# Kernel optimization log

Measured on AMD Instinct MI355X. Metric: run time of the kernel, lower is better.

Reference implementation:

```python
import jax, jax.numpy as jnp
import numpy as np

N_REP = 8      # N: repeated gelu(LN(linear)) blocks
M_LAYERS = 4   # M: transformer encoder layers
SEQ = 100
D = 4
FF = 2048      # PyTorch TransformerEncoderLayer default dim_feedforward
H = 4          # nhead; head_dim = 1


def _ln(x, g, b, axes):
    m = jnp.mean(x, axis=axes, keepdims=True)
    v = jnp.var(x, axis=axes, keepdims=True)
    return (x - m) / jnp.sqrt(v + 1e-5) * g + b


def _encoder_layer(x, Win, bi, Wout, bout, W1, b1, W2, b2, g1, be1, g2, be2):
    # x: [S, Nb, D] with S = batch_size (batch_first=False!), Nb = 100
    S, Nb, E = x.shape
    qkv = x @ Win.T + bi                      # [S, Nb, 3D]
    q, k, v = jnp.split(qkv, 3, axis=-1)
    qh = q.reshape(S, Nb, H, E // H)          # head_dim = 1, scale 1/sqrt(1)=1
    kh = k.reshape(S, Nb, H, E // H)
    vh = v.reshape(S, Nb, H, E // H)
    scores = jnp.einsum('snhd,tnhd->nhst', qh, kh)   # [Nb, H, S, S]
    attn = jax.nn.softmax(scores, axis=-1)
    o = jnp.einsum('nhst,tnhd->snhd', attn, vh).reshape(S, Nb, E)
    o = o @ Wout.T + bout
    x = _ln(x + o, g1, be1, (-1,))            # post-norm (norm_first=False)
    f = jax.nn.relu(x @ W1.T + b1) @ W2.T + b2
    return _ln(x + f, g2, be2, (-1,))


def setup_inputs() -> dict:
    key = jax.random.key(0)
    ks = jax.random.split(key, 24)
    B = 256
    d = {}
    d['x'] = jax.random.normal(ks[0], (B, SEQ, D), dtype=jnp.float32)
    # conv1: kernel_size=1, 1->1 channel -> scalar affine
    d['conv_w'] = jax.random.normal(ks[1], (), dtype=jnp.float32) * 0.5 + 1.0
    d['conv_b'] = jax.random.normal(ks[2], (), dtype=jnp.float32) * 0.1
    # shared 4x4 linear (self.liner) and LayerNorm([100,4])
    d['Wl'] = jax.random.normal(ks[3], (D, D), dtype=jnp.float32) * 0.5
    d['bl'] = jax.random.normal(ks[4], (D,), dtype=jnp.float32) * 0.1
    d['ln_g'] = jnp.ones((SEQ, D), dtype=jnp.float32)
    d['ln_b'] = jnp.zeros((SEQ, D), dtype=jnp.float32)
    # transformer encoder params, stacked over M layers
    s = 0.3
    d['Win'] = jax.random.normal(ks[5], (M_LAYERS, 3 * D, D), dtype=jnp.float32) * s
    d['bi'] = jax.random.normal(ks[6], (M_LAYERS, 3 * D), dtype=jnp.float32) * 0.05
    d['Wout'] = jax.random.normal(ks[7], (M_LAYERS, D, D), dtype=jnp.float32) * s
    d['bout'] = jax.random.normal(ks[8], (M_LAYERS, D), dtype=jnp.float32) * 0.05
    d['W1'] = jax.random.normal(ks[9], (M_LAYERS, FF, D), dtype=jnp.float32) * 0.05
    d['b1'] = jax.random.normal(ks[10], (M_LAYERS, FF), dtype=jnp.float32) * 0.05
    d['W2'] = jax.random.normal(ks[11], (M_LAYERS, D, FF), dtype=jnp.float32) * 0.02
    d['b2'] = jax.random.normal(ks[12], (M_LAYERS, D), dtype=jnp.float32) * 0.05
    d['g1'] = jnp.ones((M_LAYERS, D), dtype=jnp.float32)
    d['be1'] = jnp.zeros((M_LAYERS, D), dtype=jnp.float32)
    d['g2'] = jnp.ones((M_LAYERS, D), dtype=jnp.float32)
    d['be2'] = jnp.zeros((M_LAYERS, D), dtype=jnp.float32)
    return d


def reference(x, conv_w, conv_b, Wl, bl, ln_g, ln_b,
              Win, bi, Wout, bout, W1, b1, W2, b2, g1, be1, g2, be2):
    # per-channel kernel_size=1 conv == elementwise affine (same scalar for all 4 channels)
    h = x * conv_w + conv_b                   # [B, 100, 4]
    for _ in range(N_REP):
        h = jax.nn.gelu(_ln(h @ Wl.T + bl, ln_g, ln_b, (-2, -1)), approximate=False)
    h = h @ Wl.T + bl
    for i in range(M_LAYERS):
        h = _encoder_layer(h, Win[i], bi[i], Wout[i], bout[i], W1[i], b1[i],
                           W2[i], b2[i], g1[i], be1[i], g2[i], be2[i])
    h = h @ Wl.T + bl
    return jax.nn.softmax(h, axis=2)
```

## Files before the change

kernel.cpp:

```cpp
#include <hip/hip_runtime.h>
#include <math.h>

#define SEQ   100
#define BATCH 256
#define NREP  8
#define FFD   2048
#define RSQRT2 0.70710678118654752440f

__device__ __forceinline__ float wsum(float v) {
#pragma unroll
  for (int o = 32; o > 0; o >>= 1) v += __shfl_xor(v, o, 64);
  return v;
}

__global__ __launch_bounds__(64) void k_stageA(
    const float* __restrict__ x, const float* __restrict__ convw,
    const float* __restrict__ convb, const float* __restrict__ Wl,
    const float* __restrict__ bl, const float* __restrict__ lng,
    const float* __restrict__ lnb, float* __restrict__ XT)
{
  const int b = blockIdx.x;
  const int lane = threadIdx.x;
  const bool act = lane < 50;

  const float cw = convw[0], cb = convb[0];
  float W[4][4], B[4];
#pragma unroll
  for (int j = 0; j < 4; ++j) {
    B[j] = bl[j];
#pragma unroll
    for (int d = 0; d < 4; ++d) W[j][d] = Wl[j * 4 + d];
  }

  float h[2][4] = {{0.f,0.f,0.f,0.f},{0.f,0.f,0.f,0.f}};
  float gg[2][4] = {{0.f}}, eb[2][4] = {{0.f}};
  if (act) {
#pragma unroll
    for (int p = 0; p < 2; ++p) {
      const int r = lane * 2 + p;
      float4 xr = *(const float4*)(x + (b * SEQ + r) * 4);
      h[p][0] = fmaf(xr.x, cw, cb); h[p][1] = fmaf(xr.y, cw, cb);
      h[p][2] = fmaf(xr.z, cw, cb); h[p][3] = fmaf(xr.w, cw, cb);
      float4 gv = *(const float4*)(lng + r * 4);
      float4 bv = *(const float4*)(lnb + r * 4);
      gg[p][0] = gv.x; gg[p][1] = gv.y; gg[p][2] = gv.z; gg[p][3] = gv.w;
      eb[p][0] = bv.x; eb[p][1] = bv.y; eb[p][2] = bv.z; eb[p][3] = bv.w;
    }
  }
  for (int it = 0; it < NREP; ++it) {
    float y[2][4] = {{0.f,0.f,0.f,0.f},{0.f,0.f,0.f,0.f}};
    float s1 = 0.f, s2 = 0.f;
    if (act) {
#pragma unroll
      for (int p = 0; p < 2; ++p)
#pragma unroll
        for (int j = 0; j < 4; ++j) {
          float yy = B[j];
#pragma unroll
          for (int d = 0; d < 4; ++d) yy = fmaf(h[p][d], W[j][d], yy);
          y[p][j] = yy; s1 += yy; s2 = fmaf(yy, yy, s2);
        }
    }
    s1 = wsum(s1); s2 = wsum(s2);
    const float mean = s1 * (1.0f / 400.0f);
    const float var  = s2 * (1.0f / 400.0f) - mean * mean;
    const float rstd = rsqrtf(var + 1e-5f);
    if (act) {
#pragma unroll
      for (int p = 0; p < 2; ++p)
#pragma unroll
        for (int j = 0; j < 4; ++j) {
          float vv = fmaf((y[p][j] - mean) * rstd, gg[p][j], eb[p][j]);
          h[p][j] = 0.5f * vv * (1.0f + erff(vv * RSQRT2));
        }
    }
  }
  if (act) {
#pragma unroll
    for (int p = 0; p < 2; ++p) {
      const int r = lane * 2 + p;
      float yy[4];
#pragma unroll
      for (int j = 0; j < 4; ++j) {
        float a = B[j];
#pragma unroll
        for (int d = 0; d < 4; ++d) a = fmaf(h[p][d], W[j][d], a);
        yy[j] = a;
      }
      *(float4*)(XT + (r * BATCH + b) * 4) =
          make_float4(yy[0], yy[1], yy[2], yy[3]);
    }
  }
}

__global__ __launch_bounds__(512) void k_layer(
    const float* __restrict__ XTin, float* __restrict__ XTout,
    const float* __restrict__ Wa,  const float* __restrict__ ba,
    const float* __restrict__ Wo,  const float* __restrict__ bo,
    const float* __restrict__ W1l, const float* __restrict__ b1l,
    const float* __restrict__ W2l, const float* __restrict__ b2l,
    const float* __restrict__ g1l, const float* __restrict__ e1l,
    const float* __restrict__ g2l, const float* __restrict__ e2l,
    const float* __restrict__ Wl,  const float* __restrict__ bl,
    float* __restrict__ out, const int last)
{
  const int n      = blockIdx.x;
  const int base_s = blockIdx.y * 128;
  const int t      = threadIdx.x;
  const int lane   = t & 63;
  const int wv     = t >> 6;
  const int h      = t >> 7;
  const int qr     = t & 127;

  __shared__ float2 kv[4][256];
  __shared__ float  osm[4][128];
  __shared__ float  x1s[128][4];
  __shared__ float  pacc[8][128][4];
  __shared__ float  kred[8][2];

  if (t < 256) {
    float4 xr = *(const float4*)(XTin + (n * BATCH + t) * 4);
#pragma unroll
    for (int hh = 0; hh < 4; ++hh) {
      const float* wk = Wa + (4 + hh) * 4;
      const float* wp = Wa + (8 + hh) * 4;
      float k = ba[4+hh] + xr.x*wk[0] + xr.y*wk[1] + xr.z*wk[2] + xr.w*wk[3];
      float v = ba[8+hh] + xr.x*wp[0] + xr.y*wp[1] + xr.z*wp[2] + xr.w*wp[3];
      kv[hh][t] = make_float2(k, v);
    }
  }
  float q;
  {
    float4 xr = *(const float4*)(XTin + (n * BATCH + base_s + qr) * 4);
    const float* wq = Wa + h * 4;
    q = ba[h] + xr.x*wq[0] + xr.y*wq[1] + xr.z*wq[2] + xr.w*wq[3];
  }
  __syncthreads();

  {
    float a = kv[h][qr].x, c = kv[h][qr + 128].x;
    float mx = fmaxf(a, c), mn = fminf(a, c);
#pragma unroll
    for (int o = 32; o > 0; o >>= 1) {
      mx = fmaxf(mx, __shfl_xor(mx, o, 64));
      mn = fminf(mn, __shfl_xor(mn, o, 64));
    }
    if (lane == 0) { kred[wv][0] = mx; kred[wv][1] = mn; }
  }
  __syncthreads();

  {
    const float kmx = fmaxf(kred[2*h][0], kred[2*h+1][0]);
    const float kmn = fminf(kred[2*h][1], kred[2*h+1][1]);
    const float m = (q >= 0.f) ? q * kmx : q * kmn;
    float den0 = 0.f, den1 = 0.f, num0 = 0.f, num1 = 0.f;
#pragma unroll 4
    for (int t2 = 0; t2 < 256; t2 += 2) {
      float4 kk = *(const float4*)&kv[h][t2];
      float p0 = __expf(fmaf(q, kk.x, -m));
      float p1 = __expf(fmaf(q, kk.z, -m));
      den0 += p0; num0 = fmaf(p0, kk.y, num0);
      den1 += p1; num1 = fmaf(p1, kk.w, num1);
    }
    osm[h][qr] = (num0 + num1) / (den0 + den1);
  }
  __syncthreads();

  {
    const int r = t >> 2, d = t & 3;
    const int g = n * BATCH + base_s + r;
    const float o0 = osm[0][r], o1 = osm[1][r], o2 = osm[2][r], o3 = osm[3][r];
    float rr = XTin[g * 4 + d] + bo[d]
             + o0 * Wo[d*4+0] + o1 * Wo[d*4+1] + o2 * Wo[d*4+2] + o3 * Wo[d*4+3];
    float sum = rr + __shfl_xor(rr, 1, 64); sum += __shfl_xor(sum, 2, 64);
    const float mean = 0.25f * sum;
    const float dv = rr - mean;
    float qq = dv * dv;
    float qs = qq + __shfl_xor(qq, 1, 64); qs += __shfl_xor(qs, 2, 64);
    const float rstd = rsqrtf(0.25f * qs + 1e-5f);
    x1s[r][d] = fmaf(dv * rstd, g1l[d], e1l[d]);
  }
  __syncthreads();

  {
    const int fb = __builtin_amdgcn_readfirstlane(wv) * 256;
    const float xA0 = x1s[lane][0], xA1 = x1s[lane][1];
    const float xA2 = x1s[lane][2], xA3 = x1s[lane][3];
    const float xB0 = x1s[64+lane][0], xB1 = x1s[64+lane][1];
    const float xB2 = x1s[64+lane][2], xB3 = x1s[64+lane][3];
    float aA0=0.f,aA1=0.f,aA2=0.f,aA3=0.f;
    float aB0=0.f,aB1=0.f,aB2=0.f,aB3=0.f;
#pragma unroll 4
    for (int j = 0; j < 256; ++j) {
      const int f = fb + j;
      const float4 w1 = *(const float4*)(W1l + f * 4);
      const float bb  = b1l[f];
      const float w20 = W2l[f],           w21 = W2l[FFD + f];
      const float w22 = W2l[2*FFD + f],   w23 = W2l[3*FFD + f];
      float hA = fmaf(xA3, w1.w, fmaf(xA2, w1.z, fmaf(xA1, w1.y, fmaf(xA0, w1.x, bb))));
      hA = fmaxf(hA, 0.f);
      aA0 = fmaf(hA, w20, aA0); aA1 = fmaf(hA, w21, aA1);
      aA2 = fmaf(hA, w22, aA2); aA3 = fmaf(hA, w23, aA3);
      float hB = fmaf(xB3, w1.w, fmaf(xB2, w1.z, fmaf(xB1, w1.y, fmaf(xB0, w1.x, bb))));
      hB = fmaxf(hB, 0.f);
      aB0 = fmaf(hB, w20, aB0); aB1 = fmaf(hB, w21, aB1);
      aB2 = fmaf(hB, w22, aB2); aB3 = fmaf(hB, w23, aB3);
    }
    *(float4*)&pacc[wv][lane][0]      = make_float4(aA0, aA1, aA2, aA3);
    *(float4*)&pacc[wv][64 + lane][0] = make_float4(aB0, aB1, aB2, aB3);
  }
  __syncthreads();

  {
    const int r = t >> 2, d = t & 3;
    float s8 = b2l[d];
#pragma unroll
    for (int w = 0; w < 8; ++w) s8 += pacc[w][r][d];
    float val = x1s[r][d] + s8;
    float sum = val + __shfl_xor(val, 1, 64); sum += __shfl_xor(sum, 2, 64);
    const float mean = 0.25f * sum;
    const float dv = val - mean;
    float qq = dv * dv;
    float qs = qq + __shfl_xor(qq, 1, 64); qs += __shfl_xor(qs, 2, 64);
    const float rstd = rsqrtf(0.25f * qs + 1e-5f);
    const float res = fmaf(dv * rstd, g2l[d], e2l[d]);
    if (!last) XTout[(n * BATCH + base_s + r) * 4 + d] = res;
    else       x1s[r][d] = res;
  }

  if (last) {
    __syncthreads();
    const int r = t >> 2, j = t & 3;
    const float y = fmaf(x1s[r][3], Wl[j*4+3], fmaf(x1s[r][2], Wl[j*4+2],
                    fmaf(x1s[r][1], Wl[j*4+1], fmaf(x1s[r][0], Wl[j*4+0], bl[j]))));
    float mx = fmaxf(y, __shfl_xor(y, 1, 64)); mx = fmaxf(mx, __shfl_xor(mx, 2, 64));
    const float e = __expf(y - mx);
    float se = e + __shfl_xor(e, 1, 64); se += __shfl_xor(se, 2, 64);
    out[((base_s + r) * SEQ + n) * 4 + j] = e / se;
  }
}

extern "C" void kernel_launch(void* const* d_in, const int* in_sizes, int n_in,
                              void* d_out, int out_size, void* d_ws, size_t ws_size,
                              hipStream_t stream)
{
  const float* x     = (const float*)d_in[0];
  const float* convw = (const float*)d_in[1];
  const float* convb = (const float*)d_in[2];
  const float* Wl    = (const float*)d_in[3];
  const float* bl    = (const float*)d_in[4];
  const float* lng   = (const float*)d_in[5];
  const float* lnb   = (const float*)d_in[6];
  const float* Win   = (const float*)d_in[7];
  const float* bi    = (const float*)d_in[8];
  const float* Wout  = (const float*)d_in[9];
  const float* bout  = (const float*)d_in[10];
  const float* W1    = (const float*)d_in[11];
  const float* b1    = (const float*)d_in[12];
  const float* W2    = (const float*)d_in[13];
  const float* b2    = (const float*)d_in[14];
  const float* g1    = (const float*)d_in[15];
  const float* be1   = (const float*)d_in[16];
  const float* g2    = (const float*)d_in[17];
  const float* be2   = (const float*)d_in[18];

  float* XT0 = (float*)d_ws;
  float* XT1 = XT0 + SEQ * BATCH * 4;

  k_stageA<<<BATCH, 64, 0, stream>>>(x, convw, convb, Wl, bl, lng, lnb, XT0);
  for (int l = 0; l < 4; ++l) {
    const float* in  = (l & 1) ? XT1 : XT0;
    float*       outb= (l & 1) ? XT0 : XT1;
    k_layer<<<dim3(SEQ, 2), 512, 0, stream>>>(
        in, outb,
        Win + l * 48, bi + l * 12, Wout + l * 16, bout + l * 4,
        W1 + l * FFD * 4, b1 + l * FFD, W2 + l * 4 * FFD, b2 + l * 4,
        g1 + l * 4, be1 + l * 4, g2 + l * 4, be2 + l * 4,
        Wl, bl, (float*)d_out, (l == 3) ? 1 : 0);
  }
}
```

Before: 132.6 us.

## Stage FFN weights through shared memory with register prefetch in encoder kernel

The FFN loop used to read W1/b1/W2 straight from global memory in each wave, with each wave covering 256 features. It now loads a 512-feature chunk cooperatively into an LDS buffer, prefetching the next chunk into registers while the current one is computed, and each wave handles 64 features per chunk. The KV projection is split across all 512 threads, and the softmax loop is unrolled with four independent accumulators. This adds about 24KB of LDS and 8 extra block barriers, which may reduce occupancy.

```diff
diff --git a/kernel.cpp b/kernel.cpp
--- a/kernel.cpp
+++ b/kernel.cpp
@@ -112,21 +112,33 @@
   const int h      = t >> 7;
   const int qr     = t & 127;
 
+  __shared__ __align__(16) float wbuf[512][12];
   __shared__ float2 kv[4][256];
   __shared__ float  osm[4][128];
   __shared__ float  x1s[128][4];
   __shared__ float  pacc[8][128][4];
   __shared__ float  kred[8][2];
 
-  if (t < 256) {
-    float4 xr = *(const float4*)(XTin + (n * BATCH + t) * 4);
-#pragma unroll
-    for (int hh = 0; hh < 4; ++hh) {
+  float4 s_w1; float s_b1, s_w20, s_w21, s_w22, s_w23;
+  {
+    const int f = t;
+    s_w1  = *(const float4*)(W1l + f * 4);
+    s_b1  = b1l[f];
+    s_w20 = W2l[f];           s_w21 = W2l[FFD + f];
+    s_w22 = W2l[2 * FFD + f]; s_w23 = W2l[3 * FFD + f];
+  }
+
+  {
+    const int s = t & 255, pr = t >> 8;
+    float4 xr = *(const float4*)(XTin + (n * BATCH + s) * 4);
+#pragma unroll
+    for (int i = 0; i < 2; ++i) {
+      const int hh = pr * 2 + i;
       const float* wk = Wa + (4 + hh) * 4;
       const float* wp = Wa + (8 + hh) * 4;
       float k = ba[4+hh] + xr.x*wk[0] + xr.y*wk[1] + xr.z*wk[2] + xr.w*wk[3];
       float v = ba[8+hh] + xr.x*wp[0] + xr.y*wp[1] + xr.z*wp[2] + xr.w*wp[3];
-      kv[hh][t] = make_float2(k, v);
+      kv[hh][s] = make_float2(k, v);
     }
   }
   float q;
@@ -153,16 +165,23 @@
     const float kmx = fmaxf(kred[2*h][0], kred[2*h+1][0]);
     const float kmn = fminf(kred[2*h][1], kred[2*h+1][1]);
     const float m = (q >= 0.f) ? q * kmx : q * kmn;
-    float den0 = 0.f, den1 = 0.f, num0 = 0.f, num1 = 0.f;
+    float d0=0.f,d1=0.f,d2=0.f,d3=0.f,n0=0.f,n1=0.f,n2=0.f,n3=0.f;
 #pragma unroll 4
-    for (int t2 = 0; t2 < 256; t2 += 2) {
-      float4 kk = *(const float4*)&kv[h][t2];
-      float p0 = __expf(fmaf(q, kk.x, -m));
-      float p1 = __expf(fmaf(q, kk.z, -m));
-      den0 += p0; num0 = fmaf(p0, kk.y, num0);
-      den1 += p1; num1 = fmaf(p1, kk.w, num1);
-    }
-    osm[h][qr] = (num0 + num1) / (den0 + den1);
+    for (int t2 = 0; t2 < 256; t2 += 8) {
+      float4 a = *(const float4*)&kv[h][t2];
+      float4 b = *(const float4*)&kv[h][t2+2];
+      float4 c = *(const float4*)&kv[h][t2+4];
+      float4 e = *(const float4*)&kv[h][t2+6];
+      float p0 = __expf(fmaf(q, a.x, -m)); d0 += p0; n0 = fmaf(p0, a.y, n0);
+      float p1 = __expf(fmaf(q, a.z, -m)); d1 += p1; n1 = fmaf(p1, a.w, n1);
+      float p2 = __expf(fmaf(q, b.x, -m)); d2 += p2; n2 = fmaf(p2, b.y, n2);
+      float p3 = __expf(fmaf(q, b.z, -m)); d3 += p3; n3 = fmaf(p3, b.w, n3);
+      p0 = __expf(fmaf(q, c.x, -m)); d0 += p0; n0 = fmaf(p0, c.y, n0);
+      p1 = __expf(fmaf(q, c.z, -m)); d1 += p1; n1 = fmaf(p1, c.w, n1);
+      p2 = __expf(fmaf(q, e.x, -m)); d2 += p2; n2 = fmaf(p2, e.y, n2);
+      p3 = __expf(fmaf(q, e.z, -m)); d3 += p3; n3 = fmaf(p3, e.w, n3);
+    }
+    osm[h][qr] = (n0+n1+n2+n3) / (d0+d1+d2+d3);
   }
   __syncthreads();
 
@@ -182,33 +201,45 @@
   }
   __syncthreads();
 
-  {
-    const int fb = __builtin_amdgcn_readfirstlane(wv) * 256;
-    const float xA0 = x1s[lane][0], xA1 = x1s[lane][1];
-    const float xA2 = x1s[lane][2], xA3 = x1s[lane][3];
-    const float xB0 = x1s[64+lane][0], xB1 = x1s[64+lane][1];
-    const float xB2 = x1s[64+lane][2], xB3 = x1s[64+lane][3];
-    float aA0=0.f,aA1=0.f,aA2=0.f,aA3=0.f;
-    float aB0=0.f,aB1=0.f,aB2=0.f,aB3=0.f;
+  const float xA0 = x1s[lane][0],    xA1 = x1s[lane][1];
+  const float xA2 = x1s[lane][2],    xA3 = x1s[lane][3];
+  const float xB0 = x1s[64+lane][0], xB1 = x1s[64+lane][1];
+  const float xB2 = x1s[64+lane][2], xB3 = x1s[64+lane][3];
+  float aA0=0.f,aA1=0.f,aA2=0.f,aA3=0.f;
+  float aB0=0.f,aB1=0.f,aB2=0.f,aB3=0.f;
+
+  for (int p = 0; p < 4; ++p) {
+    __syncthreads();
+    *(float4*)&wbuf[t][0] = s_w1;
+    *(float4*)&wbuf[t][4] = make_float4(s_b1, s_w20, s_w21, s_w22);
+    wbuf[t][8] = s_w23;
+    if (p < 3) {
+      const int f = (p + 1) * 512 + t;
+      s_w1  = *(const float4*)(W1l + f * 4);
+      s_b1  = b1l[f];
+      s_w20 = W2l[f];           s_w21 = W2l[FFD + f];
+      s_w22 = W2l[2 * FFD + f]; s_w23 = W2l[3 * FFD + f];
+    }
+    __syncthreads();
+    const int fb = wv * 64;
 #pragma unroll 4
-    for (int j = 0; j < 256; ++j) {
-      const int f = fb + j;
-      const float4 w1 = *(const float4*)(W1l + f * 4);
-      const float bb  = b1l[f];
-      const float w20 = W2l[f],           w21 = W2l[FFD + f];
-      const float w22 = W2l[2*FFD + f],   w23 = W2l[3*FFD + f];
-      float hA = fmaf(xA3, w1.w, fmaf(xA2, w1.z, fmaf(xA1, w1.y, fmaf(xA0, w1.x, bb))));
+    for (int j = 0; j < 64; ++j) {
+      const int fl = fb + j;
+      const float4 w1 = *(const float4*)&wbuf[fl][0];
+      const float4 wb = *(const float4*)&wbuf[fl][4];
+      const float w23 = wbuf[fl][8];
+      float hA = fmaf(xA3, w1.w, fmaf(xA2, w1.z, fmaf(xA1, w1.y, fmaf(xA0, w1.x, wb.x))));
       hA = fmaxf(hA, 0.f);
-      aA0 = fmaf(hA, w20, aA0); aA1 = fmaf(hA, w21, aA1);
-      aA2 = fmaf(hA, w22, aA2); aA3 = fmaf(hA, w23, aA3);
-      float hB = fmaf(xB3, w1.w, fmaf(xB2, w1.z, fmaf(xB1, w1.y, fmaf(xB0, w1.x, bb))));
+      aA0 = fmaf(hA, wb.y, aA0); aA1 = fmaf(hA, wb.z, aA1);
+      aA2 = fmaf(hA, wb.w, aA2); aA3 = fmaf(hA, w23, aA3);
+      float hB = fmaf(xB3, w1.w, fmaf(xB2, w1.z, fmaf(xB1, w1.y, fmaf(xB0, w1.x, wb.x))));
       hB = fmaxf(hB, 0.f);
-      aB0 = fmaf(hB, w20, aB0); aB1 = fmaf(hB, w21, aB1);
-      aB2 = fmaf(hB, w22, aB2); aB3 = fmaf(hB, w23, aB3);
-    }
-    *(float4*)&pacc[wv][lane][0]      = make_float4(aA0, aA1, aA2, aA3);
-    *(float4*)&pacc[wv][64 + lane][0] = make_float4(aB0, aB1, aB2, aB3);
-  }
+      aB0 = fmaf(hB, wb.y, aB0); aB1 = fmaf(hB, wb.z, aB1);
+      aB2 = fmaf(hB, wb.w, aB2); aB3 = fmaf(hB, w23, aB3);
+    }
+  }
+  *(float4*)&pacc[wv][lane][0]      = make_float4(aA0, aA1, aA2, aA3);
+  *(float4*)&pacc[wv][64 + lane][0] = make_float4(aB0, aB1, aB2, aB3);
   __syncthreads();
 
   {
```

Result: faster. 121.7 us (-8.2%).

## Double block size, split attention keys, and restructure FFN with transposed W2

Applied to the files above, without the earlier changes.

Each layer block grows from 512 to 1024 threads. Attention now splits the 256 keys into four chunks per head, and each thread handles two query rows; the partial sums are combined through shared memory. The FFN loop changes from each wave owning a slice of FF for all 128 rows to each wave owning 8 rows, with lanes striding over FF. This lets a W2 value loaded once be reused across 8 rows, read as float4 from a W2 layout transposed by a new prep kernel, and the results are combined by wave reductions. The change adds an extra kernel launch, extra shuffle reductions and more register pressure, and half the threads sit idle in the epilogue phases.

```diff
diff --git a/kernel.cpp b/kernel.cpp
--- a/kernel.cpp
+++ b/kernel.cpp
@@ -11,6 +11,15 @@
 #pragma unroll
   for (int o = 32; o > 0; o >>= 1) v += __shfl_xor(v, o, 64);
   return v;
+}
+
+__global__ __launch_bounds__(256) void k_prep(
+    const float* __restrict__ W2, float* __restrict__ W2T)
+{
+  const int id = blockIdx.x * 256 + threadIdx.x;
+  const float* src = W2 + (id >> 11) * 4 * FFD + (id & 2047);
+  *(float4*)(W2T + id * 4) =
+      make_float4(src[0], src[FFD], src[2 * FFD], src[3 * FFD]);
 }
 
 __global__ __launch_bounds__(64) void k_stageA(
@@ -31,7 +40,6 @@
 #pragma unroll
     for (int d = 0; d < 4; ++d) W[j][d] = Wl[j * 4 + d];
   }
-
   float h[2][4] = {{0.f,0.f,0.f,0.f},{0.f,0.f,0.f,0.f}};
   float gg[2][4] = {{0.f}}, eb[2][4] = {{0.f}};
   if (act) {
@@ -93,12 +101,12 @@
   }
 }
 
-__global__ __launch_bounds__(512) void k_layer(
+__global__ __launch_bounds__(1024, 4) void k_layer(
     const float* __restrict__ XTin, float* __restrict__ XTout,
     const float* __restrict__ Wa,  const float* __restrict__ ba,
     const float* __restrict__ Wo,  const float* __restrict__ bo,
     const float* __restrict__ W1l, const float* __restrict__ b1l,
-    const float* __restrict__ W2l, const float* __restrict__ b2l,
+    const float* __restrict__ W2Tl,const float* __restrict__ b2l,
     const float* __restrict__ g1l, const float* __restrict__ e1l,
     const float* __restrict__ g2l, const float* __restrict__ e2l,
     const float* __restrict__ Wl,  const float* __restrict__ bl,
@@ -109,69 +117,85 @@
   const int t      = threadIdx.x;
   const int lane   = t & 63;
   const int wv     = t >> 6;
-  const int h      = t >> 7;
-  const int qr     = t & 127;
-
-  __shared__ float2 kv[4][256];
+  const int ah     = wv & 3;
+  const int kq     = wv >> 2;
+
+  __shared__ __align__(16) float2 kv[4][256];
+  __shared__ float2 part[4][128][5];
   __shared__ float  osm[4][128];
   __shared__ float  x1s[128][4];
-  __shared__ float  pacc[8][128][4];
-  __shared__ float  kred[8][2];
-
-  if (t < 256) {
-    float4 xr = *(const float4*)(XTin + (n * BATCH + t) * 4);
-#pragma unroll
-    for (int hh = 0; hh < 4; ++hh) {
-      const float* wk = Wa + (4 + hh) * 4;
-      const float* wp = Wa + (8 + hh) * 4;
-      float k = ba[4+hh] + xr.x*wk[0] + xr.y*wk[1] + xr.z*wk[2] + xr.w*wk[3];
-      float v = ba[8+hh] + xr.x*wp[0] + xr.y*wp[1] + xr.z*wp[2] + xr.w*wp[3];
-      kv[hh][t] = make_float2(k, v);
-    }
-  }
-  float q;
-  {
-    float4 xr = *(const float4*)(XTin + (n * BATCH + base_s + qr) * 4);
-    const float* wq = Wa + h * 4;
-    q = ba[h] + xr.x*wq[0] + xr.y*wq[1] + xr.z*wq[2] + xr.w*wq[3];
-  }
-  __syncthreads();
-
-  {
-    float a = kv[h][qr].x, c = kv[h][qr + 128].x;
-    float mx = fmaxf(a, c), mn = fminf(a, c);
+  __shared__ float  fout[128][4];
+  __shared__ float2 kred[4][4];
+
+  {
+    const int s = t & 255, hh = t >> 8;
+    float4 xr = *(const float4*)(XTin + (n * BATCH + s) * 4);
+    const float* wk = Wa + (4 + hh) * 4;
+    const float* wp = Wa + (8 + hh) * 4;
+    float k = ba[4+hh] + xr.x*wk[0] + xr.y*wk[1] + xr.z*wk[2] + xr.w*wk[3];
+    float v = ba[8+hh] + xr.x*wp[0] + xr.y*wp[1] + xr.z*wp[2] + xr.w*wp[3];
+    kv[hh][s] = make_float2(k, v);
+  }
+  float q0, q1;
+  {
+    const float* wq = Wa + ah * 4;
+    float4 xa = *(const float4*)(XTin + (n * BATCH + base_s + 2 * lane) * 4);
+    float4 xb = *(const float4*)(XTin + (n * BATCH + base_s + 2 * lane + 1) * 4);
+    q0 = ba[ah] + xa.x*wq[0] + xa.y*wq[1] + xa.z*wq[2] + xa.w*wq[3];
+    q1 = ba[ah] + xb.x*wq[0] + xb.y*wq[1] + xb.z*wq[2] + xb.w*wq[3];
+  }
+  __syncthreads();
+
+  {
+    float k = kv[ah][kq * 64 + lane].x;
+    float mx = k, mn = k;
 #pragma unroll
     for (int o = 32; o > 0; o >>= 1) {
       mx = fmaxf(mx, __shfl_xor(mx, o, 64));
       mn = fminf(mn, __shfl_xor(mn, o, 64));
     }
-    if (lane == 0) { kred[wv][0] = mx; kred[wv][1] = mn; }
-  }
-  __syncthreads();
-
-  {
-    const float kmx = fmaxf(kred[2*h][0], kred[2*h+1][0]);
-    const float kmn = fminf(kred[2*h][1], kred[2*h+1][1]);
-    const float m = (q >= 0.f) ? q * kmx : q * kmn;
-    float den0 = 0.f, den1 = 0.f, num0 = 0.f, num1 = 0.f;
+    if (lane == 0) kred[ah][kq] = make_float2(mx, mn);
+  }
+  __syncthreads();
+
+  {
+    const float kmx = fmaxf(fmaxf(kred[ah][0].x, kred[ah][1].x),
+                            fmaxf(kred[ah][2].x, kred[ah][3].x));
+    const float kmn = fminf(fminf(kred[ah][0].y, kred[ah][1].y),
+                            fminf(kred[ah][2].y, kred[ah][3].y));
+    const float m0 = (q0 >= 0.f) ? q0 * kmx : q0 * kmn;
+    const float m1 = (q1 >= 0.f) ? q1 * kmx : q1 * kmn;
+    const int kb = kq * 64;
+    float dA = 0.f, nA = 0.f, dB = 0.f, nB = 0.f;
 #pragma unroll 4
-    for (int t2 = 0; t2 < 256; t2 += 2) {
-      float4 kk = *(const float4*)&kv[h][t2];
-      float p0 = __expf(fmaf(q, kk.x, -m));
-      float p1 = __expf(fmaf(q, kk.z, -m));
-      den0 += p0; num0 = fmaf(p0, kk.y, num0);
-      den1 += p1; num1 = fmaf(p1, kk.w, num1);
-    }
-    osm[h][qr] = (num0 + num1) / (den0 + den1);
-  }
-  __syncthreads();
-
-  {
+    for (int i = 0; i < 32; ++i) {
+      const int p = ((lane + i) & 31) * 2;
+      float4 kk = *(const float4*)&kv[ah][kb + p];
+      float pA0 = __expf(fmaf(q0, kk.x, -m0));
+      float pA1 = __expf(fmaf(q0, kk.z, -m0));
+      float pB0 = __expf(fmaf(q1, kk.x, -m1));
+      float pB1 = __expf(fmaf(q1, kk.z, -m1));
+      dA += pA0 + pA1; nA = fmaf(pA1, kk.w, fmaf(pA0, kk.y, nA));
+      dB += pB0 + pB1; nB = fmaf(pB1, kk.w, fmaf(pB0, kk.y, nB));
+    }
+    part[ah][2 * lane][kq]     = make_float2(dA, nA);
+    part[ah][2 * lane + 1][kq] = make_float2(dB, nB);
+  }
+  __syncthreads();
+
+  if (t < 512) {
+    const int h = t >> 7, qr = t & 127;
+    float2 a = part[h][qr][0], b = part[h][qr][1];
+    float2 c = part[h][qr][2], d = part[h][qr][3];
+    osm[h][qr] = (a.y + b.y + c.y + d.y) / (a.x + b.x + c.x + d.x);
+  }
+  __syncthreads();
+
+  if (t < 512) {
     const int r = t >> 2, d = t & 3;
-    const int g = n * BATCH + base_s + r;
     const float o0 = osm[0][r], o1 = osm[1][r], o2 = osm[2][r], o3 = osm[3][r];
-    float rr = XTin[g * 4 + d] + bo[d]
-             + o0 * Wo[d*4+0] + o1 * Wo[d*4+1] + o2 * Wo[d*4+2] + o3 * Wo[d*4+3];
+    float rr = XTin[(n * BATCH + base_s + r) * 4 + d] + bo[d]
+             + o0*Wo[d*4+0] + o1*Wo[d*4+1] + o2*Wo[d*4+2] + o3*Wo[d*4+3];
     float sum = rr + __shfl_xor(rr, 1, 64); sum += __shfl_xor(sum, 2, 64);
     const float mean = 0.25f * sum;
     const float dv = rr - mean;
@@ -183,40 +207,57 @@
   __syncthreads();
 
   {
-    const int fb = __builtin_amdgcn_readfirstlane(wv) * 256;
-    const float xA0 = x1s[lane][0], xA1 = x1s[lane][1];
-    const float xA2 = x1s[lane][2], xA3 = x1s[lane][3];
-    const float xB0 = x1s[64+lane][0], xB1 = x1s[64+lane][1];
-    const float xB2 = x1s[64+lane][2], xB3 = x1s[64+lane][3];
-    float aA0=0.f,aA1=0.f,aA2=0.f,aA3=0.f;
-    float aB0=0.f,aB1=0.f,aB2=0.f,aB3=0.f;
+    const int r0 = wv * 8;
+    float xr[8][4];
+#pragma unroll
+    for (int rr = 0; rr < 8; ++rr) {
+      float4 v = *(const float4*)&x1s[r0 + rr][0];
+      xr[rr][0] = v.x; xr[rr][1] = v.y; xr[rr][2] = v.z; xr[rr][3] = v.w;
+    }
+    float acc[8][4] = {{0.f,0.f,0.f,0.f},{0.f,0.f,0.f,0.f},
+                       {0.f,0.f,0.f,0.f},{0.f,0.f,0.f,0.f},
+                       {0.f,0.f,0.f,0.f},{0.f,0.f,0.f,0.f},
+                       {0.f,0.f,0.f,0.f},{0.f,0.f,0.f,0.f}};
+    const float* w1p = W1l + lane * 4;
+    const float* w2p = W2Tl + lane * 4;
+    const float* b1p = b1l + lane;
 #pragma unroll 4
-    for (int j = 0; j < 256; ++j) {
-      const int f = fb + j;
-      const float4 w1 = *(const float4*)(W1l + f * 4);
-      const float bb  = b1l[f];
-      const float w20 = W2l[f],           w21 = W2l[FFD + f];
-      const float w22 = W2l[2*FFD + f],   w23 = W2l[3*FFD + f];
-      float hA = fmaf(xA3, w1.w, fmaf(xA2, w1.z, fmaf(xA1, w1.y, fmaf(xA0, w1.x, bb))));
-      hA = fmaxf(hA, 0.f);
-      aA0 = fmaf(hA, w20, aA0); aA1 = fmaf(hA, w21, aA1);
-      aA2 = fmaf(hA, w22, aA2); aA3 = fmaf(hA, w23, aA3);
-      float hB = fmaf(xB3, w1.w, fmaf(xB2, w1.z, fmaf(xB1, w1.y, fmaf(xB0, w1.x, bb))));
-      hB = fmaxf(hB, 0.f);
-      aB0 = fmaf(hB, w20, aB0); aB1 = fmaf(hB, w21, aB1);
-      aB2 = fmaf(hB, w22, aB2); aB3 = fmaf(hB, w23, aB3);
-    }
-    *(float4*)&pacc[wv][lane][0]      = make_float4(aA0, aA1, aA2, aA3);
-    *(float4*)&pacc[wv][64 + lane][0] = make_float4(aB0, aB1, aB2, aB3);
-  }
-  __syncthreads();
-
-  {
+    for (int j = 0; j < 32; ++j) {
+      const float4 w1 = *(const float4*)(w1p + j * 256);
+      const float4 w2 = *(const float4*)(w2p + j * 256);
+      const float  bb = b1p[j * 64];
+#pragma unroll
+      for (int rr = 0; rr < 8; ++rr) {
+        float hh = fmaf(xr[rr][3], w1.w, fmaf(xr[rr][2], w1.z,
+                   fmaf(xr[rr][1], w1.y, fmaf(xr[rr][0], w1.x, bb))));
+        hh = fmaxf(hh, 0.f);
+        acc[rr][0] = fmaf(hh, w2.x, acc[rr][0]);
+        acc[rr][1] = fmaf(hh, w2.y, acc[rr][1]);
+        acc[rr][2] = fmaf(hh, w2.z, acc[rr][2]);
+        acc[rr][3] = fmaf(hh, w2.w, acc[rr][3]);
+      }
+    }
+#pragma unroll
+    for (int rr = 0; rr < 8; ++rr)
+#pragma unroll
+      for (int d = 0; d < 4; ++d) {
+        float v = acc[rr][d];
+#pragma unroll
+        for (int o = 32; o > 0; o >>= 1) v += __shfl_xor(v, o, 64);
+        acc[rr][d] = v;
+      }
+    if (lane == 0) {
+#pragma unroll
+      for (int rr = 0; rr < 8; ++rr)
+        *(float4*)&fout[r0 + rr][0] =
+            make_float4(acc[rr][0], acc[rr][1], acc[rr][2], acc[rr][3]);
+    }
+  }
+  __syncthreads();
+
+  if (t < 512) {
     const int r = t >> 2, d = t & 3;
-    float s8 = b2l[d];
-#pragma unroll
-    for (int w = 0; w < 8; ++w) s8 += pacc[w][r][d];
-    float val = x1s[r][d] + s8;
+    float val = x1s[r][d] + fout[r][d] + b2l[d];
     float sum = val + __shfl_xor(val, 1, 64); sum += __shfl_xor(sum, 2, 64);
     const float mean = 0.25f * sum;
     const float dv = val - mean;
@@ -230,13 +271,15 @@
 
   if (last) {
     __syncthreads();
-    const int r = t >> 2, j = t & 3;
-    const float y = fmaf(x1s[r][3], Wl[j*4+3], fmaf(x1s[r][2], Wl[j*4+2],
-                    fmaf(x1s[r][1], Wl[j*4+1], fmaf(x1s[r][0], Wl[j*4+0], bl[j]))));
-    float mx = fmaxf(y, __shfl_xor(y, 1, 64)); mx = fmaxf(mx, __shfl_xor(mx, 2, 64));
-    const float e = __expf(y - mx);
-    float se = e + __shfl_xor(e, 1, 64); se += __shfl_xor(se, 2, 64);
-    out[((base_s + r) * SEQ + n) * 4 + j] = e / se;
+    if (t < 512) {
+      const int r = t >> 2, j = t & 3;
+      const float y = fmaf(x1s[r][3], Wl[j*4+3], fmaf(x1s[r][2], Wl[j*4+2],
+                      fmaf(x1s[r][1], Wl[j*4+1], fmaf(x1s[r][0], Wl[j*4+0], bl[j]))));
+      float mx = fmaxf(y, __shfl_xor(y, 1, 64)); mx = fmaxf(mx, __shfl_xor(mx, 2, 64));
+      const float e = __expf(y - mx);
+      float se = e + __shfl_xor(e, 1, 64); se += __shfl_xor(se, 2, 64);
+      out[((base_s + r) * SEQ + n) * 4 + j] = e / se;
+    }
   }
 }
 
@@ -266,15 +309,17 @@
 
   float* XT0 = (float*)d_ws;
   float* XT1 = XT0 + SEQ * BATCH * 4;
-
+  float* W2T = XT1 + SEQ * BATCH * 4;
+
+  k_prep<<<32, 256, 0, stream>>>(W2, W2T);
   k_stageA<<<BATCH, 64, 0, stream>>>(x, convw, convb, Wl, bl, lng, lnb, XT0);
   for (int l = 0; l < 4; ++l) {
     const float* in  = (l & 1) ? XT1 : XT0;
     float*       outb= (l & 1) ? XT0 : XT1;
-    k_layer<<<dim3(SEQ, 2), 512, 0, stream>>>(
+    k_layer<<<dim3(SEQ, 2), 1024, 0, stream>>>(
         in, outb,
         Win + l * 48, bi + l * 12, Wout + l * 16, bout + l * 4,
-        W1 + l * FFD * 4, b1 + l * FFD, W2 + l * 4 * FFD, b2 + l * 4,
+        W1 + l * FFD * 4, b1 + l * FFD, W2T + l * FFD * 4, b2 + l * 4,
         g1 + l * 4, be1 + l * 4, g2 + l * 4, be2 + l * 4,
         Wl, bl, (float*)d_out, (l == 3) ? 1 : 0);
   }
```

Result: no change. 134.1 us (+1.2%).

## Split layer into attention and FFN kernels with packed FFN weights

Applied to the files above, without the earlier changes.

Splits each encoder layer into two kernels. The attention kernel is gridded over sequence and head. The FFN kernel is gridded over 256 row-blocks of 100 tokens with 1024 threads, and each wave covers 128 hidden units. A prep kernel repacks W1, W2 and b1 into contiguous 36-float groups so each FFN weight group can be read as uniform contiguous loads. The change also adds an extra launch per layer, an intermediate O buffer and a one-time prep pass, and 14 of 64 lanes sit idle in the FFN loop.

```diff
diff --git a/kernel.cpp b/kernel.cpp
--- a/kernel.cpp
+++ b/kernel.cpp
@@ -13,6 +13,26 @@
   return v;
 }
 
+__global__ __launch_bounds__(256) void k_prep(
+    const float* __restrict__ W1, const float* __restrict__ b1,
+    const float* __restrict__ W2, float* __restrict__ Wp)
+{
+  const int id = blockIdx.x * 256 + threadIdx.x;
+  const int l = id >> 9, g = id & 511, f0 = g * 4;
+  float* dst = Wp + id * 36;
+  const float* w1 = W1 + (l * FFD + f0) * 4;
+#pragma unroll
+  for (int i = 0; i < 16; ++i) dst[i] = w1[i];
+  const float* w2 = W2 + l * 4 * FFD;
+#pragma unroll
+  for (int f = 0; f < 4; ++f)
+#pragma unroll
+    for (int d = 0; d < 4; ++d) dst[16 + f * 4 + d] = w2[d * FFD + f0 + f];
+  const float* bb = b1 + l * FFD + f0;
+#pragma unroll
+  for (int f = 0; f < 4; ++f) dst[32 + f] = bb[f];
+}
+
 __global__ __launch_bounds__(64) void k_stageA(
     const float* __restrict__ x, const float* __restrict__ convw,
     const float* __restrict__ convb, const float* __restrict__ Wl,
@@ -31,7 +51,6 @@
 #pragma unroll
     for (int d = 0; d < 4; ++d) W[j][d] = Wl[j * 4 + d];
   }
-
   float h[2][4] = {{0.f,0.f,0.f,0.f},{0.f,0.f,0.f,0.f}};
   float gg[2][4] = {{0.f}}, eb[2][4] = {{0.f}};
   if (act) {
@@ -93,130 +112,140 @@
   }
 }
 
-__global__ __launch_bounds__(512) void k_layer(
-    const float* __restrict__ XTin, float* __restrict__ XTout,
-    const float* __restrict__ Wa,  const float* __restrict__ ba,
+__global__ __launch_bounds__(128) void k_attn(
+    const float* __restrict__ XT, float* __restrict__ O,
+    const float* __restrict__ Wa, const float* __restrict__ ba)
+{
+  const int n  = blockIdx.x;
+  const int hd = blockIdx.y;
+  const int t  = threadIdx.x;
+  const int wid = t >> 6;
+  __shared__ float2 kvs[256];
+  __shared__ float  red[2][2];
+
+  float4 xa = *(const float4*)(XT + (n * BATCH + t) * 4);
+  float4 xb = *(const float4*)(XT + (n * BATCH + t + 128) * 4);
+  const float* wq = Wa + hd * 4;
+  const float* wk = Wa + (4 + hd) * 4;
+  const float* wv = Wa + (8 + hd) * 4;
+  const float bq = ba[hd], bk = ba[4 + hd], bv = ba[8 + hd];
+  float q0 = bq + xa.x*wq[0] + xa.y*wq[1] + xa.z*wq[2] + xa.w*wq[3];
+  float q1 = bq + xb.x*wq[0] + xb.y*wq[1] + xb.z*wq[2] + xb.w*wq[3];
+  float k0 = bk + xa.x*wk[0] + xa.y*wk[1] + xa.z*wk[2] + xa.w*wk[3];
+  float k1 = bk + xb.x*wk[0] + xb.y*wk[1] + xb.z*wk[2] + xb.w*wk[3];
+  float v0 = bv + xa.x*wv[0] + xa.y*wv[1] + xa.z*wv[2] + xa.w*wv[3];
+  float v1 = bv + xb.x*wv[0] + xb.y*wv[1] + xb.z*wv[2] + xb.w*wv[3];
+  kvs[t]       = make_float2(k0, v0);
+  kvs[t + 128] = make_float2(k1, v1);
+
+  float mx = fmaxf(k0, k1), mn = fminf(k0, k1);
+#pragma unroll
+  for (int o = 32; o > 0; o >>= 1) {
+    mx = fmaxf(mx, __shfl_xor(mx, o, 64));
+    mn = fminf(mn, __shfl_xor(mn, o, 64));
+  }
+  if ((t & 63) == 0) { red[wid][0] = mx; red[wid][1] = mn; }
+  __syncthreads();
+  const float kmx = fmaxf(red[0][0], red[1][0]);
+  const float kmn = fminf(red[0][1], red[1][1]);
+
+  const float m0 = (q0 >= 0.f) ? q0 * kmx : q0 * kmn;
+  const float m1 = (q1 >= 0.f) ? q1 * kmx : q1 * kmn;
+  float dA = 0.f, nA = 0.f, dB = 0.f, nB = 0.f;
+#pragma unroll 4
+  for (int i = 0; i < 128; ++i) {
+    float4 kk = ((const float4*)kvs)[i];
+    float pA0 = __expf(fmaf(q0, kk.x, -m0));
+    float pA1 = __expf(fmaf(q0, kk.z, -m0));
+    float pB0 = __expf(fmaf(q1, kk.x, -m1));
+    float pB1 = __expf(fmaf(q1, kk.z, -m1));
+    dA += pA0 + pA1; nA = fmaf(pA1, kk.w, fmaf(pA0, kk.y, nA));
+    dB += pB0 + pB1; nB = fmaf(pB1, kk.w, fmaf(pB0, kk.y, nB));
+  }
+  O[(n * BATCH + t) * 4 + hd]       = nA / dA;
+  O[(n * BATCH + t + 128) * 4 + hd] = nB / dB;
+}
+
+__global__ __launch_bounds__(1024) void k_ffn(
+    float* __restrict__ XT, const float* __restrict__ O,
     const float* __restrict__ Wo,  const float* __restrict__ bo,
-    const float* __restrict__ W1l, const float* __restrict__ b1l,
-    const float* __restrict__ W2l, const float* __restrict__ b2l,
+    const float* __restrict__ Wpl, const float* __restrict__ b2l,
     const float* __restrict__ g1l, const float* __restrict__ e1l,
     const float* __restrict__ g2l, const float* __restrict__ e2l,
     const float* __restrict__ Wl,  const float* __restrict__ bl,
     float* __restrict__ out, const int last)
 {
-  const int n      = blockIdx.x;
-  const int base_s = blockIdx.y * 128;
-  const int t      = threadIdx.x;
-  const int lane   = t & 63;
-  const int wv     = t >> 6;
-  const int h      = t >> 7;
-  const int qr     = t & 127;
-
-  __shared__ float2 kv[4][256];
-  __shared__ float  osm[4][128];
-  __shared__ float  x1s[128][4];
-  __shared__ float  pacc[8][128][4];
-  __shared__ float  kred[8][2];
-
-  if (t < 256) {
-    float4 xr = *(const float4*)(XTin + (n * BATCH + t) * 4);
-#pragma unroll
-    for (int hh = 0; hh < 4; ++hh) {
-      const float* wk = Wa + (4 + hh) * 4;
-      const float* wp = Wa + (8 + hh) * 4;
-      float k = ba[4+hh] + xr.x*wk[0] + xr.y*wk[1] + xr.z*wk[2] + xr.w*wk[3];
-      float v = ba[8+hh] + xr.x*wp[0] + xr.y*wp[1] + xr.z*wp[2] + xr.w*wp[3];
-      kv[hh][t] = make_float2(k, v);
-    }
-  }
-  float q;
-  {
-    float4 xr = *(const float4*)(XTin + (n * BATCH + base_s + qr) * 4);
-    const float* wq = Wa + h * 4;
-    q = ba[h] + xr.x*wq[0] + xr.y*wq[1] + xr.z*wq[2] + xr.w*wq[3];
-  }
-  __syncthreads();
-
-  {
-    float a = kv[h][qr].x, c = kv[h][qr + 128].x;
-    float mx = fmaxf(a, c), mn = fminf(a, c);
-#pragma unroll
-    for (int o = 32; o > 0; o >>= 1) {
-      mx = fmaxf(mx, __shfl_xor(mx, o, 64));
-      mn = fminf(mn, __shfl_xor(mn, o, 64));
-    }
-    if (lane == 0) { kred[wv][0] = mx; kred[wv][1] = mn; }
-  }
-  __syncthreads();
-
-  {
-    const float kmx = fmaxf(kred[2*h][0], kred[2*h+1][0]);
-    const float kmn = fminf(kred[2*h][1], kred[2*h+1][1]);
-    const float m = (q >= 0.f) ? q * kmx : q * kmn;
-    float den0 = 0.f, den1 = 0.f, num0 = 0.f, num1 = 0.f;
-#pragma unroll 4
-    for (int t2 = 0; t2 < 256; t2 += 2) {
-      float4 kk = *(const float4*)&kv[h][t2];
-      float p0 = __expf(fmaf(q, kk.x, -m));
-      float p1 = __expf(fmaf(q, kk.z, -m));
-      den0 += p0; num0 = fmaf(p0, kk.y, num0);
-      den1 += p1; num1 = fmaf(p1, kk.w, num1);
-    }
-    osm[h][qr] = (num0 + num1) / (den0 + den1);
-  }
-  __syncthreads();
-
-  {
-    const int r = t >> 2, d = t & 3;
-    const int g = n * BATCH + base_s + r;
-    const float o0 = osm[0][r], o1 = osm[1][r], o2 = osm[2][r], o3 = osm[3][r];
-    float rr = XTin[g * 4 + d] + bo[d]
-             + o0 * Wo[d*4+0] + o1 * Wo[d*4+1] + o2 * Wo[d*4+2] + o3 * Wo[d*4+3];
+  const int b    = blockIdx.x;
+  const int t    = threadIdx.x;
+  const int lane = t & 63;
+  const int wv   = t >> 6;
+
+  __shared__ float x1s[100][4];
+  __shared__ float pacc[16][100][4];
+
+  if (t < 400) {
+    const int j = t >> 2, d = t & 3;
+    const int i = b * 100 + j;
+    const float xd = XT[i * 4 + d];
+    float4 o4 = *(const float4*)(O + i * 4);
+    float rr = xd + bo[d] + o4.x*Wo[d*4+0] + o4.y*Wo[d*4+1]
+                          + o4.z*Wo[d*4+2] + o4.w*Wo[d*4+3];
     float sum = rr + __shfl_xor(rr, 1, 64); sum += __shfl_xor(sum, 2, 64);
     const float mean = 0.25f * sum;
     const float dv = rr - mean;
     float qq = dv * dv;
     float qs = qq + __shfl_xor(qq, 1, 64); qs += __shfl_xor(qs, 2, 64);
     const float rstd = rsqrtf(0.25f * qs + 1e-5f);
-    x1s[r][d] = fmaf(dv * rstd, g1l[d], e1l[d]);
+    x1s[j][d] = fmaf(dv * rstd, g1l[d], e1l[d]);
   }
   __syncthreads();
 
   {
-    const int fb = __builtin_amdgcn_readfirstlane(wv) * 256;
-    const float xA0 = x1s[lane][0], xA1 = x1s[lane][1];
-    const float xA2 = x1s[lane][2], xA3 = x1s[lane][3];
-    const float xB0 = x1s[64+lane][0], xB1 = x1s[64+lane][1];
-    const float xB2 = x1s[64+lane][2], xB3 = x1s[64+lane][3];
+    const int wvu = __builtin_amdgcn_readfirstlane(wv);
+    const float* __restrict__ gp0 = Wpl + (wvu * 32) * 36;
+    const int j0 = (lane < 50) ? lane : 0;
+    const int j1 = (lane < 50) ? lane + 50 : 0;
+    const float4 xA = *(const float4*)&x1s[j0][0];
+    const float4 xB = *(const float4*)&x1s[j1][0];
     float aA0=0.f,aA1=0.f,aA2=0.f,aA3=0.f;
     float aB0=0.f,aB1=0.f,aB2=0.f,aB3=0.f;
-#pragma unroll 4
-    for (int j = 0; j < 256; ++j) {
-      const int f = fb + j;
-      const float4 w1 = *(const float4*)(W1l + f * 4);
-      const float bb  = b1l[f];
-      const float w20 = W2l[f],           w21 = W2l[FFD + f];
-      const float w22 = W2l[2*FFD + f],   w23 = W2l[3*FFD + f];
-      float hA = fmaf(xA3, w1.w, fmaf(xA2, w1.z, fmaf(xA1, w1.y, fmaf(xA0, w1.x, bb))));
-      hA = fmaxf(hA, 0.f);
-      aA0 = fmaf(hA, w20, aA0); aA1 = fmaf(hA, w21, aA1);
-      aA2 = fmaf(hA, w22, aA2); aA3 = fmaf(hA, w23, aA3);
-      float hB = fmaf(xB3, w1.w, fmaf(xB2, w1.z, fmaf(xB1, w1.y, fmaf(xB0, w1.x, bb))));
-      hB = fmaxf(hB, 0.f);
-      aB0 = fmaf(hB, w20, aB0); aB1 = fmaf(hB, w21, aB1);
-      aB2 = fmaf(hB, w22, aB2); aB3 = fmaf(hB, w23, aB3);
-    }
-    *(float4*)&pacc[wv][lane][0]      = make_float4(aA0, aA1, aA2, aA3);
-    *(float4*)&pacc[wv][64 + lane][0] = make_float4(aB0, aB1, aB2, aB3);
+#pragma unroll 2
+    for (int g = 0; g < 32; ++g) {
+      const float* gp = gp0 + g * 36;
+      float w[36];
+#pragma unroll
+      for (int i = 0; i < 36; ++i) w[i] = gp[i];
+#pragma unroll
+      for (int f = 0; f < 4; ++f) {
+        const float w10 = w[f*4+0], w11 = w[f*4+1];
+        const float w12 = w[f*4+2], w13 = w[f*4+3];
+        const float w20 = w[16+f*4+0], w21 = w[16+f*4+1];
+        const float w22 = w[16+f*4+2], w23 = w[16+f*4+3];
+        const float bb  = w[32+f];
+        float hA = fmaf(xA.w, w13, fmaf(xA.z, w12, fmaf(xA.y, w11, fmaf(xA.x, w10, bb))));
+        hA = fmaxf(hA, 0.f);
+        aA0 = fmaf(hA, w20, aA0); aA1 = fmaf(hA, w21, aA1);
+        aA2 = fmaf(hA, w22, aA2); aA3 = fmaf(hA, w23, aA3);
+        float hB = fmaf(xB.w, w13, fmaf(xB.z, w12, fmaf(xB.y, w11, fmaf(xB.x, w10, bb))));
+        hB = fmaxf(hB, 0.f);
+        aB0 = fmaf(hB, w20, aB0); aB1 = fmaf(hB, w21, aB1);
+        aB2 = fmaf(hB, w22, aB2); aB3 = fmaf(hB, w23, aB3);
+      }
+    }
+    if (lane < 50) {
+      *(float4*)&pacc[wv][lane][0]      = make_float4(aA0, aA1, aA2, aA3);
+      *(float4*)&pacc[wv][lane + 50][0] = make_float4(aB0, aB1, aB2, aB3);
+    }
   }
   __syncthreads();
 
-  {
-    const int r = t >> 2, d = t & 3;
-    float s8 = b2l[d];
-#pragma unroll
-    for (int w = 0; w < 8; ++w) s8 += pacc[w][r][d];
-    float val = x1s[r][d] + s8;
+  if (t < 400) {
+    const int j = t >> 2, d = t & 3;
+    const int i = b * 100 + j;
+    float s16 = b2l[d];
+#pragma unroll
+    for (int w2 = 0; w2 < 16; ++w2) s16 += pacc[w2][j][d];
+    float val = x1s[j][d] + s16;
     float sum = val + __shfl_xor(val, 1, 64); sum += __shfl_xor(sum, 2, 64);
     const float mean = 0.25f * sum;
     const float dv = val - mean;
@@ -224,19 +253,24 @@
     float qs = qq + __shfl_xor(qq, 1, 64); qs += __shfl_xor(qs, 2, 64);
     const float rstd = rsqrtf(0.25f * qs + 1e-5f);
     const float res = fmaf(dv * rstd, g2l[d], e2l[d]);
-    if (!last) XTout[(n * BATCH + base_s + r) * 4 + d] = res;
-    else       x1s[r][d] = res;
-  }
-
-  if (last) {
-    __syncthreads();
-    const int r = t >> 2, j = t & 3;
-    const float y = fmaf(x1s[r][3], Wl[j*4+3], fmaf(x1s[r][2], Wl[j*4+2],
-                    fmaf(x1s[r][1], Wl[j*4+1], fmaf(x1s[r][0], Wl[j*4+0], bl[j]))));
-    float mx = fmaxf(y, __shfl_xor(y, 1, 64)); mx = fmaxf(mx, __shfl_xor(mx, 2, 64));
-    const float e = __expf(y - mx);
-    float se = e + __shfl_xor(e, 1, 64); se += __shfl_xor(se, 2, 64);
-    out[((base_s + r) * SEQ + n) * 4 + j] = e / se;
+    if (!last) {
+      XT[i * 4 + d] = res;
+    } else {
+      float y0 = Wl[0*4+d] * res, y1 = Wl[1*4+d] * res;
+      float y2 = Wl[2*4+d] * res, y3 = Wl[3*4+d] * res;
+      y0 += __shfl_xor(y0, 1, 64); y0 += __shfl_xor(y0, 2, 64);
+      y1 += __shfl_xor(y1, 1, 64); y1 += __shfl_xor(y1, 2, 64);
+      y2 += __shfl_xor(y2, 1, 64); y2 += __shfl_xor(y2, 2, 64);
+      y3 += __shfl_xor(y3, 1, 64); y3 += __shfl_xor(y3, 2, 64);
+      y0 += bl[0]; y1 += bl[1]; y2 += bl[2]; y3 += bl[3];
+      const float mxy = fmaxf(fmaxf(y0, y1), fmaxf(y2, y3));
+      const float e0 = __expf(y0 - mxy), e1 = __expf(y1 - mxy);
+      const float e2 = __expf(y2 - mxy), e3 = __expf(y3 - mxy);
+      const float inv = 1.0f / (e0 + e1 + e2 + e3);
+      const float ee = (d == 0) ? e0 : (d == 1) ? e1 : (d == 2) ? e2 : e3;
+      const int s = i & 255, nn = i >> 8;
+      out[(s * SEQ + nn) * 4 + d] = ee * inv;
+    }
   }
 }
 
@@ -264,17 +298,17 @@
   const float* g2    = (const float*)d_in[17];
   const float* be2   = (const float*)d_in[18];
 
-  float* XT0 = (float*)d_ws;
-  float* XT1 = XT0 + SEQ * BATCH * 4;
-
-  k_stageA<<<BATCH, 64, 0, stream>>>(x, convw, convb, Wl, bl, lng, lnb, XT0);
+  float* XT = (float*)d_ws;
+  float* O  = XT + SEQ * BATCH * 4;
+  float* Wp = O + SEQ * BATCH * 4;
+
+  k_prep<<<8, 256, 0, stream>>>(W1, b1, W2, Wp);
+  k_stageA<<<BATCH, 64, 0, stream>>>(x, convw, convb, Wl, bl, lng, lnb, XT);
   for (int l = 0; l < 4; ++l) {
-    const float* in  = (l & 1) ? XT1 : XT0;
-    float*       outb= (l & 1) ? XT0 : XT1;
-    k_layer<<<dim3(SEQ, 2), 512, 0, stream>>>(
-        in, outb,
-        Win + l * 48, bi + l * 12, Wout + l * 16, bout + l * 4,
-        W1 + l * FFD * 4, b1 + l * FFD, W2 + l * 4 * FFD, b2 + l * 4,
+    k_attn<<<dim3(SEQ, 4), 128, 0, stream>>>(XT, O, Win + l * 48, bi + l * 12);
+    k_ffn<<<256, 1024, 0, stream>>>(
+        XT, O, Wout + l * 16, bout + l * 4,
+        Wp + l * 512 * 36, b2 + l * 4,
         g1 + l * 4, be1 + l * 4, g2 + l * 4, be2 + l * 4,
         Wl, bl, (float*)d_out, (l == 3) ? 1 : 0);
   }
```

After: 140.2 us. 1.06x slower.
